# Kernel tuning notes

Measured on AMD Instinct MI355X. Metric: run time of the kernel, lower is better.

## Reference

```python
import jax, jax.numpy as jnp
import numpy as np

B, T, D, N, H = 1, 256, 512, 8, 64  # batch, seq, d_model, n_heads, d_head
INIT_STD = 0.02
IGNORE = -1000000.0
DUMMY_LOGIT = -1000.0


def setup_inputs() -> dict:
    key = jax.random.key(0)
    ks = jax.random.split(key, 9)
    std = INIT_STD
    inp = {
        'normalized_resid_pre': jax.random.normal(ks[0], (B, T, D), dtype=jnp.float32),
        'W_K1': jax.random.normal(ks[1], (N, D, H), dtype=jnp.float32) * std,
        'W_K2': jax.random.normal(ks[2], (N, D, H), dtype=jnp.float32) * std,
        'W_Q':  jax.random.normal(ks[3], (N, D, H), dtype=jnp.float32) * std,
        'W_V1': jax.random.normal(ks[4], (N, D, H), dtype=jnp.float32) * std,
        'W_V2': jax.random.normal(ks[5], (N, D, H), dtype=jnp.float32) * std,
        'W_Kq': jax.random.normal(ks[6], (N, H, H, H), dtype=jnp.float32) * std,
        'W_Vq': jax.random.normal(ks[7], (N, H, H, H), dtype=jnp.float32) * std,
        'W_O':  jax.random.normal(ks[8], (N, H, D), dtype=jnp.float32) * std,
        'b_K1': jnp.zeros((N, H), dtype=jnp.float32),
        'b_K2': jnp.zeros((N, H), dtype=jnp.float32),
        'b_Q':  jnp.zeros((N, H), dtype=jnp.float32),
        'b_V1': jnp.zeros((N, H), dtype=jnp.float32),
        'b_V2': jnp.zeros((N, H), dtype=jnp.float32),
        'b_O':  jnp.zeros((D,), dtype=jnp.float32),
    }
    return inp


def _trittention(x, W_K1, W_K2, W_Q, W_V1, W_V2, W_Kq, W_Vq, W_O,
                 b_K1, b_K2, b_Q, b_V1, b_V2, b_O):
    b, t, d = x.shape
    n, _, h = W_Q.shape
    proj = lambda W, bias: jnp.einsum('ndh,bpd->bpnh', W, x) + bias
    k1 = proj(W_K1, b_K1)  # (b, t, n, h)
    k2 = proj(W_K2, b_K2)
    q  = proj(W_Q,  b_Q)
    v1 = proj(W_V1, b_V1)
    v2 = proj(W_V2, b_V2)

    # bilinear value over pairs of positions: (b, n, h, s, t) -> flatten (s t)
    v = jnp.einsum('bsni,btnj,nijh->bnhst', v1, v2, W_Vq)
    v = v.reshape(b, n, h, t * t)

    # cubic scores: (b, n, s, t, r) with s=k1 pos, t=k2 pos, r=query pos
    step1 = jnp.einsum('brnk,nijk->bnrij', q, W_Kq)
    step2 = jnp.einsum('bnrij,btnj->bnrit', step1, k2)
    attn = jnp.einsum('bnrit,bsni->bnstr', step2, k1)

    # causal + ordering mask (order_attn=True, attn_eq=False):
    # masked if s>=r or t>=r or s>=t
    s_idx = jnp.arange(t)[:, None, None]
    t_idx = jnp.arange(t)[None, :, None]
    r_idx = jnp.arange(t)[None, None, :]
    mask = (s_idx >= r_idx) | (t_idx >= r_idx) | (s_idx >= t_idx)
    attn = jnp.where(mask, IGNORE, attn)

    # rearrange 'b n s t r -> b n r (s t)' and scale by d_head
    attn = jnp.transpose(attn, (0, 1, 4, 2, 3)).reshape(b, n, t, t * t) / h

    # causal_attn=True: append dummy logit / zero value slot
    dummy_logit = jnp.full((b, n, t, 1), DUMMY_LOGIT, dtype=attn.dtype)
    attn = jnp.concatenate([attn, dummy_logit], axis=-1)
    dummy_value = jnp.zeros((b, n, h, 1), dtype=v.dtype)
    v = jnp.concatenate([v, dummy_value], axis=-1)

    attn = jax.nn.softmax(attn, axis=-1)
    z = jnp.einsum('bnql,bnhl->bqnh', attn, v)
    out = jnp.einsum('bpnh,nhd->bpd', z, W_O) + b_O  # sum over heads folded in
    return out


def reference(normalized_resid_pre, W_K1, W_K2, W_Q, W_V1, W_V2, W_Kq, W_Vq, W_O,
              b_K1, b_K2, b_Q, b_V1, b_V2, b_O):
    return _trittention(normalized_resid_pre, W_K1, W_K2, W_Q, W_V1, W_V2,
                        W_Kq, W_Vq, W_O, b_K1, b_K2, b_Q, b_V1, b_V2, b_O)
```

## Files before the change

kernel.cpp:

```cpp
#include <hip/hip_runtime.h>
#include <hip/hip_bf16.h>
#include <math.h>

#define TT 256
#define DD 512
#define NN 8
#define HH 64
#define PROJ 131072

typedef __attribute__((ext_vector_type(8))) short short8v;
typedef __attribute__((ext_vector_type(4))) short short4v;
typedef __attribute__((ext_vector_type(4))) float f32x4;

__device__ __forceinline__ short f2bf(float x) {
    union { float f; unsigned u; } v; v.f = x;
    unsigned r = (v.u + 0x7FFFu + ((v.u >> 16) & 1u)) >> 16;
    return (short)r;
}

#define LGKM0 asm volatile("s_waitcnt lgkmcnt(0)" ::: "memory")

#define F_NUM  0
#define F_DEN  131072
#define F_END  133120
#define S_PB   0
#define S_XB   655360
#define S_WB   786432
#define S_KQB  2097152
#define S_VQB  4194304
#define S_WOB  6291456
#define S_S1B  6553600
#define S_AB   14942208
#define S_GB   23330816

__global__ __launch_bounds__(256) void prep_kernel(
    const float* __restrict__ x, const float* __restrict__ W_Kq,
    const float* __restrict__ W0, const float* __restrict__ W1,
    const float* __restrict__ W2, const float* __restrict__ W3,
    const float* __restrict__ W4, const float* __restrict__ Vq,
    const float* __restrict__ WO, short* __restrict__ sb, float* __restrict__ fz)
{
    __shared__ float plds[64 * 129];
    int b = blockIdx.x;
    int tid = threadIdx.x;
    if (b < 1024) {
        int i = b * 256 + tid;
        const float4 f0 = *(const float4*)(W_Kq + (size_t)i * 8);
        const float4 f1 = *(const float4*)(W_Kq + (size_t)i * 8 + 4);
        short8v o;
        o[0]=f2bf(f0.x); o[1]=f2bf(f0.y); o[2]=f2bf(f0.z); o[3]=f2bf(f0.w);
        o[4]=f2bf(f1.x); o[5]=f2bf(f1.y); o[6]=f2bf(f1.z); o[7]=f2bf(f1.w);
        *(short8v*)(sb + S_KQB + (size_t)i * 8) = o;
    } else if (b < 1088) {
        int i = (b - 1024) * 256 + tid;
        const float4 f0 = *(const float4*)(x + (size_t)i * 8);
        const float4 f1 = *(const float4*)(x + (size_t)i * 8 + 4);
        short8v o;
        o[0]=f2bf(f0.x); o[1]=f2bf(f0.y); o[2]=f2bf(f0.z); o[3]=f2bf(f0.w);
        o[4]=f2bf(f1.x); o[5]=f2bf(f1.y); o[6]=f2bf(f1.z); o[7]=f2bf(f1.w);
        *(short8v*)(sb + S_XB + (size_t)i * 8) = o;
    } else if (b < 1128) {
        int pn = b - 1088; int p = pn >> 3, n = pn & 7;
        const float* Wp = (p==0)?W0:(p==1)?W1:(p==2)?W2:(p==3)?W3:W4;
        const float* src = Wp + (size_t)n * DD * HH;
        short* dst = sb + S_WB + (size_t)pn * HH * DD;
        for (int d0 = 0; d0 < DD; d0 += 64) {
            __syncthreads();
            for (int it = 0; it < 16; ++it) {
                int m = it * 256 + tid;
                int dl = m >> 6, h = m & 63;
                plds[h * 65 + dl] = src[(size_t)(d0 + dl) * 64 + h];
            }
            __syncthreads();
            int h = tid >> 2, seg = tid & 3;
            short8v o0, o1;
            #pragma unroll
            for (int e = 0; e < 8; ++e) o0[e] = f2bf(plds[h * 65 + seg * 16 + e]);
            #pragma unroll
            for (int e = 0; e < 8; ++e) o1[e] = f2bf(plds[h * 65 + seg * 16 + 8 + e]);
            *(short8v*)(dst + (size_t)h * DD + d0 + seg * 16) = o0;
            *(short8v*)(dst + (size_t)h * DD + d0 + seg * 16 + 8) = o1;
        }
    } else if (b < 1640) {
        int bb = b - 1128; int n = bb >> 6, i = bb & 63;
        const float* src = Vq + (size_t)(n * 64 + i) * 4096;
        for (int it = 0; it < 16; ++it) {
            int m = it * 256 + tid;
            int j = m >> 6, h = m & 63;
            plds[h * 65 + j] = src[(size_t)j * 64 + h];
        }
        __syncthreads();
        int h = tid >> 2, seg = tid & 3;
        short8v o0, o1;
        #pragma unroll
        for (int e = 0; e < 8; ++e) o0[e] = f2bf(plds[h * 65 + seg * 16 + e]);
        #pragma unroll
        for (int e = 0; e < 8; ++e) o1[e] = f2bf(plds[h * 65 + seg * 16 + 8 + e]);
        short* dst = sb + S_VQB + (size_t)n * 262144 + (size_t)h * 4096 + i * 64 + seg * 16;
        *(short8v*)dst = o0;
        *(short8v*)(dst + 8) = o1;
    } else if (b < 1672) {
        int bb = b - 1640; int dc = bb & 7, nhc = bb >> 3;
        for (int it = 0; it < 32; ++it) {
            int m = it * 256 + tid;
            int nhl = m >> 6, dl = m & 63;
            plds[dl * 129 + nhl] = WO[(size_t)(nhc * 128 + nhl) * 512 + dc * 64 + dl];
        }
        __syncthreads();
        for (int it = 0; it < 4; ++it) {
            int m = it * 256 + tid;
            int dl = m >> 4, seg = m & 15;
            short8v o;
            #pragma unroll
            for (int e = 0; e < 8; ++e) o[e] = f2bf(plds[dl * 129 + seg * 8 + e]);
            *(short8v*)(sb + S_WOB + (size_t)(dc * 64 + dl) * 512 + nhc * 128 + seg * 8) = o;
        }
    } else {
        int i = (b - 1672) * 1024 + tid * 4;
        *(float4*)(fz + i) = make_float4(0.f, 0.f, 0.f, 0.f);
    }
}

__global__ __launch_bounds__(512) void proj_kernel(
    const short* __restrict__ xb, const short* __restrict__ Wb,
    const float* __restrict__ bK1, const float* __restrict__ bK2,
    const float* __restrict__ bQ,  const float* __restrict__ bV1,
    const float* __restrict__ bV2, short* __restrict__ Pb) {
    int p = blockIdx.x, n = blockIdx.y, mhalf = blockIdx.z;
    int wv = threadIdx.x >> 6, lane = threadIdx.x & 63, g = lane >> 4, c = lane & 15;
    __shared__ short wlds[64 * 520];
    __shared__ short sbuf[8][16 * 72];
    const short* wsrc = Wb + (size_t)(p * 8 + n) * HH * DD;
    for (int it = 0; it < 8; ++it) {
        int idx = it * 512 + threadIdx.x;
        int h = idx >> 6, seg = idx & 63;
        *(short8v*)(&wlds[h * 520 + seg * 8]) = *(const short8v*)(wsrc + (size_t)h * DD + seg * 8);
    }
    __syncthreads();
    int mt = mhalf * 8 + wv;
    f32x4 acc[4];
    #pragma unroll
    for (int ct = 0; ct < 4; ++ct) acc[ct] = (f32x4){0.f, 0.f, 0.f, 0.f};
    for (int ks = 0; ks < 16; ++ks) {
        short8v a = *(const short8v*)(xb + (size_t)(mt * 16 + c) * DD + ks * 32 + g * 8);
        #pragma unroll
        for (int ct = 0; ct < 4; ++ct) {
            short8v b = *(const short8v*)(&wlds[(ct * 16 + c) * 520 + ks * 32 + g * 8]);
            acc[ct] = __builtin_amdgcn_mfma_f32_16x16x32_bf16(a, b, acc[ct], 0, 0, 0);
        }
    }
    const float* bp = (p == 0) ? bK1 : (p == 1) ? bK2 : (p == 2) ? bQ : (p == 3) ? bV1 : bV2;
    short* sbw = &sbuf[wv][0];
    #pragma unroll
    for (int ct = 0; ct < 4; ++ct) {
        float bias = bp[n * 64 + ct * 16 + c];
        #pragma unroll
        for (int m = 0; m < 4; ++m)
            sbw[(g * 4 + m) * 72 + ct * 16 + c] = f2bf(acc[ct][m] + bias);
    }
    LGKM0;
    int rl = lane & 15, sg = lane >> 4;
    short8v o0 = *(const short8v*)(&sbw[rl * 72 + sg * 16]);
    short8v o1 = *(const short8v*)(&sbw[rl * 72 + sg * 16 + 8]);
    short* dst = Pb + (size_t)p * PROJ + (size_t)(n * 256 + mt * 16 + rl) * 64 + sg * 16;
    *(short8v*)dst = o0;
    *(short8v*)(dst + 8) = o1;
}

__global__ __launch_bounds__(256) void bgemm_kernel(
    const short* __restrict__ A0, const short* __restrict__ B0, short* __restrict__ O0,
    const short* __restrict__ A1, const short* __restrict__ B1, short* __restrict__ O1) {
    int mt = blockIdx.x, n = blockIdx.y, z = blockIdx.z;
    const short* A = (z < 4) ? A0 : A1;
    const short* B = (z < 4) ? B0 : B1;
    short* out = (z < 4) ? O0 : O1;
    int cgq = z & 3;
    int wv = threadIdx.x >> 6, lane = threadIdx.x & 63, g = lane >> 4, c = lane & 15;
    __shared__ short sbuf[4][16 * 72];
    short* sbw = &sbuf[wv][0];
    const short* abase = A + ((size_t)n * 256 + mt * 16 + c) * 64 + g * 8;
    short8v a0 = *(const short8v*)abase;
    short8v a1 = *(const short8v*)(abase + 32);
    for (int cg = cgq * 16 + wv; cg < cgq * 16 + 16; cg += 4) {
        f32x4 acc[4];
        #pragma unroll
        for (int jt = 0; jt < 4; ++jt) acc[jt] = (f32x4){0.f, 0.f, 0.f, 0.f};
        const short* bb = B + ((size_t)n * 4096 + cg * 64) * 64;
        #pragma unroll
        for (int jt = 0; jt < 4; ++jt) {
            short8v b0 = *(const short8v*)(bb + (size_t)(jt * 16 + c) * 64 + g * 8);
            short8v b1 = *(const short8v*)(bb + (size_t)(jt * 16 + c) * 64 + g * 8 + 32);
            acc[jt] = __builtin_amdgcn_mfma_f32_16x16x32_bf16(a0, b0, acc[jt], 0, 0, 0);
            acc[jt] = __builtin_amdgcn_mfma_f32_16x16x32_bf16(a1, b1, acc[jt], 0, 0, 0);
        }
        LGKM0;
        #pragma unroll
        for (int jt = 0; jt < 4; ++jt)
            #pragma unroll
            for (int m = 0; m < 4; ++m)
                sbw[(g * 4 + m) * 72 + jt * 16 + c] = f2bf(acc[jt][m]);
        LGKM0;
        int rl = lane & 15, sg = lane >> 4;
        short8v o0 = *(const short8v*)(&sbw[rl * 72 + sg * 16]);
        short8v o1 = *(const short8v*)(&sbw[rl * 72 + sg * 16 + 8]);
        short* dst = out + ((size_t)n * 256 + mt * 16 + rl) * 4096 + cg * 64 + sg * 16;
        *(short8v*)dst = o0;
        *(short8v*)(dst + 8) = o1;
    }
}

__global__ __launch_bounds__(256) void gmat_kernel(const short* __restrict__ S1b,
                                                   const short* __restrict__ K2b,
                                                   short* __restrict__ G) {
    int bid = blockIdx.x;
    int n = bid & 7;
    int tt = (bid >> 3) & 15;
    int rq = bid >> 7;
    int wv = threadIdx.x >> 6, lane = threadIdx.x & 63, g = lane >> 4, c = lane & 15;
    int t0 = tt * 16;
    __shared__ short sbuf[4][16 * 68];
    short* sbw = &sbuf[wv][0];
    const short* abase = K2b + ((size_t)n * TT + t0 + c) * 64 + g * 8;
    short8v a0 = *(const short8v*)abase;
    short8v a1 = *(const short8v*)(abase + 32);
    for (int r = t0 + rq * 4 + wv; r < 256; r += 16) {
        const short* bb = S1b + ((size_t)(n * 256 + r) * 64) * 64;
        f32x4 acc[4];
        #pragma unroll
        for (int it = 0; it < 4; ++it) {
            short8v b0 = *(const short8v*)(bb + (size_t)(it * 16 + c) * 64 + g * 8);
            short8v b1 = *(const short8v*)(bb + (size_t)(it * 16 + c) * 64 + g * 8 + 32);
            acc[it] = (f32x4){0.f, 0.f, 0.f, 0.f};
            acc[it] = __builtin_amdgcn_mfma_f32_16x16x32_bf16(a0, b0, acc[it], 0, 0, 0);
            acc[it] = __builtin_amdgcn_mfma_f32_16x16x32_bf16(a1, b1, acc[it], 0, 0, 0);
        }
        LGKM0;
        #pragma unroll
        for (int it = 0; it < 4; ++it)
            #pragma unroll
            for (int m = 0; m < 4; ++m)
                sbw[(g * 4 + m) * 68 + it * 16 + c] = f2bf(acc[it][m]);
        LGKM0;
        int trow = lane >> 2, seg = (lane & 3) * 16;
        short8v o0 = *(const short8v*)(&sbw[trow * 68 + seg]);
        short8v o1 = *(const short8v*)(&sbw[trow * 68 + seg + 8]);
        short* dst = G + (((size_t)(n * TT + t0 + trow)) * TT + r) * 64 + seg;
        *(short8v*)dst = o0;
        *(short8v*)(dst + 8) = o1;
    }
}

__global__ __launch_bounds__(1024) void attn_kernel(
    const short* __restrict__ K1b, const short* __restrict__ V1b,
    const short* __restrict__ Gm, const short* __restrict__ Ab,
    float* __restrict__ num, float* __restrict__ den)
{
    int bid = blockIdx.x;
    int n = bid & 7;
    int rest = bid >> 3;
    int pair = rest >> 2;
    int sig = rest & 3;
    int tid = threadIdx.x;
    int wv = tid >> 6, lane = tid & 63, g = lane >> 4, c = lane & 15;

    __shared__ short k1lds[64 * 72];
    __shared__ short v1lds[64 * 72];
    __shared__ short u_lds[2][64 * 68];

    int t0H = (31 - pair) * 8;
    int stmaxK = (t0H + 6) >> 4;
    int cntK = (stmaxK >= sig) ? ((stmaxK - sig) >> 2) + 1 : 0;
    for (int idx = tid; idx < cntK * 128; idx += 1024) {
        int row = idx >> 3, seg = idx & 7;
        int s = (sig + (row >> 4) * 4) * 16 + (row & 15);
        *(short8v*)(&k1lds[row * 72 + seg * 8]) =
            *(const short8v*)(K1b + ((size_t)n * TT + s) * 64 + seg * 8);
        *(short8v*)(&v1lds[row * 72 + seg * 8]) =
            *(const short8v*)(V1b + ((size_t)n * TT + s) * 64 + seg * 8);
    }
    __syncthreads();

    f32x4 numacc[4];
    #pragma unroll
    for (int b = 0; b < 4; ++b) numacc[b] = (f32x4){0.f, 0.f, 0.f, 0.f};
    float denacc = 0.f;
    int rt = wv;
    int ubuf = 0;

    for (int part = 0; part < 2; ++part) {
        int t0 = part ? t0H : pair * 8;
        for (int th = 0; th < 8; ++th) {
            int t = t0 + th;
            if (t < 1 || t > 254) continue;
            int rt_start = (t + 1) >> 4;
            int stmaxU = (t - 1) >> 4;
            int cntU = (stmaxU >= sig) ? ((stmaxU - sig) >> 2) + 1 : 0;
            if (cntU == 0) continue;

            bool valid = (rt >= rt_start);
            short8v gf0, gf1;
            if (valid) {
                const short* gb = Gm + (((size_t)(n * TT + t) * TT) + rt * 16 + c) * 64 + g * 8;
                gf0 = *(const short8v*)gb;
                gf1 = *(const short8v*)(gb + 32);
            }

            short* uw = &u_lds[ubuf][0];
            if (wv < cntU * 4) {
                int loc = wv >> 2, hs = wv & 3;
                const short* vr = &v1lds[(loc * 16 + c) * 72 + g * 8];
                short8v vf0 = *(const short8v*)vr;
                short8v vf1 = *(const short8v*)(vr + 32);
                const short* ar = Ab + (size_t)(n * TT + t) * 4096 + (hs * 16 + c) * 64 + g * 8;
                short8v ab0 = *(const short8v*)ar;
                short8v ab1 = *(const short8v*)(ar + 32);
                f32x4 ucc = (f32x4){0.f, 0.f, 0.f, 0.f};
                ucc = __builtin_amdgcn_mfma_f32_16x16x32_bf16(vf0, ab0, ucc, 0, 0, 0);
                ucc = __builtin_amdgcn_mfma_f32_16x16x32_bf16(vf1, ab1, ucc, 0, 0, 0);
                short4v uo;
                #pragma unroll
                for (int m = 0; m < 4; ++m) uo[m] = f2bf(ucc[m]);
                *(short4v*)(&uw[(hs * 16 + c) * 68 + loc * 16 + g * 4]) = uo;
            }
            __syncthreads();
            ubuf ^= 1;

            if (valid) {
                int r = rt * 16 + c;
                for (int loc = 0; loc < cntU; ++loc) {
                    int s_base = (sig + loc * 4) * 16;
                    const short* kr = &k1lds[(loc * 16 + c) * 72 + g * 8];
                    short8v af0 = *(const short8v*)kr;
                    short8v af1 = *(const short8v*)(kr + 32);
                    f32x4 lg = (f32x4){0.f, 0.f, 0.f, 0.f};
                    lg = __builtin_amdgcn_mfma_f32_16x16x32_bf16(af0, gf0, lg, 0, 0, 0);
                    lg = __builtin_amdgcn_mfma_f32_16x16x32_bf16(af1, gf1, lg, 0, 0, 0);
                    short4v eb;
                    float dsum = 0.f;
                    #pragma unroll
                    for (int m = 0; m < 4; ++m) {
                        int s = s_base + g * 4 + m;
                        float e = (s < t && r > t) ? __expf(lg[m] * 0.015625f) : 0.f;
                        dsum += e;
                        eb[m] = f2bf(e);
                    }
                    denacc += dsum;
                    #pragma unroll
                    for (int hs = 0; hs < 4; ++hs) {
                        short4v ub = *(const short4v*)(&uw[(hs * 16 + c) * 68 + loc * 16 + g * 4]);
                        numacc[hs] = __builtin_amdgcn_mfma_f32_16x16x16bf16_1k(eb, ub, numacc[hs], 0, 0, 0);
                    }
                }
            }
        }
    }

    if (__any(denacc != 0.f)) {
        float v = denacc;
        v += __shfl_xor(v, 16);
        v += __shfl_xor(v, 32);
        if (lane < 16) atomicAdd(&den[n * TT + rt * 16 + lane], v);
        #pragma unroll
        for (int hs = 0; hs < 4; ++hs)
            #pragma unroll
            for (int m = 0; m < 4; ++m)
                atomicAdd(&num[((size_t)(n * TT + rt * 16 + g * 4 + m)) * 64 + hs * 16 + c],
                          numacc[hs][m]);
    }
}

__global__ __launch_bounds__(512) void out_kernel(const float* __restrict__ num,
                                                  const float* __restrict__ den,
                                                  const short* __restrict__ WOb,
                                                  const float* __restrict__ bO,
                                                  float* __restrict__ out) {
    int mt = blockIdx.x & 15, dq = blockIdx.x >> 4;
    int wv = threadIdx.x >> 6, lane = threadIdx.x & 63, g = lane >> 4, c = lane & 15;
    int dt0 = dq * 16 + wv * 2;
    int t = mt * 16 + c;
    f32x4 acc[2];
    acc[0] = (f32x4){0.f, 0.f, 0.f, 0.f};
    acc[1] = (f32x4){0.f, 0.f, 0.f, 0.f};
    for (int ks = 0; ks < 16; ++ks) {
        int nh = ks * 32 + g * 8;
        int nn = nh >> 6, h = nh & 63;
        float dv = den[nn * 256 + t];
        float rcp = (dv > 0.f) ? 1.f / dv : 0.f;
        const float* np = num + ((size_t)(nn * 256 + t) * 64 + h);
        float4 f0 = *(const float4*)np;
        float4 f1 = *(const float4*)(np + 4);
        short8v a;
        a[0]=f2bf(f0.x*rcp); a[1]=f2bf(f0.y*rcp); a[2]=f2bf(f0.z*rcp); a[3]=f2bf(f0.w*rcp);
        a[4]=f2bf(f1.x*rcp); a[5]=f2bf(f1.y*rcp); a[6]=f2bf(f1.z*rcp); a[7]=f2bf(f1.w*rcp);
        #pragma unroll
        for (int u = 0; u < 2; ++u) {
            short8v b = *(const short8v*)(WOb + (size_t)((dt0 + u) * 16 + c) * 512 + ks * 32 + g * 8);
            acc[u] = __builtin_amdgcn_mfma_f32_16x16x32_bf16(a, b, acc[u], 0, 0, 0);
        }
    }
    #pragma unroll
    for (int u = 0; u < 2; ++u) {
        int d = (dt0 + u) * 16 + c;
        float bias = bO[d];
        #pragma unroll
        for (int m = 0; m < 4; ++m)
            out[(size_t)(mt * 16 + g * 4 + m) * 512 + d] = acc[u][m] + bias;
    }
}

extern "C" void kernel_launch(void* const* d_in, const int* in_sizes, int n_in,
                              void* d_out, int out_size, void* d_ws, size_t ws_size,
                              hipStream_t stream) {
    const float* x    = (const float*)d_in[0];
    const float* W_K1 = (const float*)d_in[1];
    const float* W_K2 = (const float*)d_in[2];
    const float* W_Q  = (const float*)d_in[3];
    const float* W_V1 = (const float*)d_in[4];
    const float* W_V2 = (const float*)d_in[5];
    const float* W_Kq = (const float*)d_in[6];
    const float* W_Vq = (const float*)d_in[7];
    const float* W_O  = (const float*)d_in[8];
    const float* b_K1 = (const float*)d_in[9];
    const float* b_K2 = (const float*)d_in[10];
    const float* b_Q  = (const float*)d_in[11];
    const float* b_V1 = (const float*)d_in[12];
    const float* b_V2 = (const float*)d_in[13];
    const float* b_O  = (const float*)d_in[14];
    float* ws = (float*)d_ws;
    short* sb = (short*)(ws + F_END);
    float* out = (float*)d_out;

    prep_kernel<<<1802, 256, 0, stream>>>(x, W_Kq, W_K1, W_K2, W_Q, W_V1, W_V2,
                                          W_Vq, W_O, sb, ws + F_NUM);

    proj_kernel<<<dim3(5, 8, 2), 512, 0, stream>>>(sb + S_XB, sb + S_WB,
                                                   b_K1, b_K2, b_Q, b_V1, b_V2, sb + S_PB);

    bgemm_kernel<<<dim3(16, 8, 8), 256, 0, stream>>>(
        sb + S_PB + 2 * PROJ, sb + S_KQB, sb + S_S1B,
        sb + S_PB + 4 * PROJ, sb + S_VQB, sb + S_AB);

    gmat_kernel<<<512, 256, 0, stream>>>(sb + S_S1B, sb + S_PB + 1 * PROJ, sb + S_GB);

    attn_kernel<<<512, 1024, 0, stream>>>(sb + S_PB, sb + S_PB + 3 * PROJ,
                                          sb + S_GB, sb + S_AB,
                                          ws + F_NUM, ws + F_DEN);

    out_kernel<<<32, 512, 0, stream>>>(ws + F_NUM, ws + F_DEN, sb + S_WOB, b_O, out);
}
```

Baseline: 146.5 us.

## Batch U-tile computation for eight t values per part to cut barriers

Instead of computing one U tile per t and syncing the block every iteration, each part now computes U tiles for all eight t values into an enlarged shared buffer, with two barriers per part. The V1 fragment is hoisted out of the loop since each wave's loc index is fixed. This removes per-t __syncthreads stalls and lets the score/accumulate loop run without barriers. In exchange shared memory for U grows about fourfold, which may reduce occupancy, and it adds a hard sync between the U phase and the attention phase.

```diff
diff --git a/kernel.cpp b/kernel.cpp
--- a/kernel.cpp
+++ b/kernel.cpp
@@ -265,7 +265,7 @@
 
     __shared__ short k1lds[64 * 72];
     __shared__ short v1lds[64 * 72];
-    __shared__ short u_lds[2][64 * 68];
+    __shared__ short u_lds[8][64][68];
 
     int t0H = (31 - pair) * 8;
     int stmaxK = (t0H + 6) >> 4;
@@ -285,71 +285,69 @@
     for (int b = 0; b < 4; ++b) numacc[b] = (f32x4){0.f, 0.f, 0.f, 0.f};
     float denacc = 0.f;
     int rt = wv;
-    int ubuf = 0;
+    int lU = wv >> 2, hU = wv & 3;
+
+    const short* vr = &v1lds[(lU * 16 + c) * 72 + g * 8];
+    short8v vf0 = *(const short8v*)vr;
+    short8v vf1 = *(const short8v*)(vr + 32);
 
     for (int part = 0; part < 2; ++part) {
         int t0 = part ? t0H : pair * 8;
-        for (int th = 0; th < 8; ++th) {
-            int t = t0 + th;
+
+        __syncthreads();
+        for (int tl = 0; tl < 8; ++tl) {
+            int t = t0 + tl;
+            int stm = (t - 1) >> 4;
+            int cntU = (t >= 1 && stm >= sig) ? ((stm - sig) >> 2) + 1 : 0;
+            if (lU >= cntU) continue;
+            const short* ar = Ab + (size_t)(n * TT + t) * 4096 + (hU * 16 + c) * 64 + g * 8;
+            short8v ab0 = *(const short8v*)ar;
+            short8v ab1 = *(const short8v*)(ar + 32);
+            f32x4 ucc = (f32x4){0.f, 0.f, 0.f, 0.f};
+            ucc = __builtin_amdgcn_mfma_f32_16x16x32_bf16(vf0, ab0, ucc, 0, 0, 0);
+            ucc = __builtin_amdgcn_mfma_f32_16x16x32_bf16(vf1, ab1, ucc, 0, 0, 0);
+            short4v uo;
+            #pragma unroll
+            for (int m = 0; m < 4; ++m) uo[m] = f2bf(ucc[m]);
+            *(short4v*)(&u_lds[tl][hU * 16 + c][lU * 16 + g * 4]) = uo;
+        }
+        __syncthreads();
+
+        for (int tl = 0; tl < 8; ++tl) {
+            int t = t0 + tl;
             if (t < 1 || t > 254) continue;
             int rt_start = (t + 1) >> 4;
             int stmaxU = (t - 1) >> 4;
             int cntU = (stmaxU >= sig) ? ((stmaxU - sig) >> 2) + 1 : 0;
-            if (cntU == 0) continue;
-
-            bool valid = (rt >= rt_start);
-            short8v gf0, gf1;
-            if (valid) {
-                const short* gb = Gm + (((size_t)(n * TT + t) * TT) + rt * 16 + c) * 64 + g * 8;
-                gf0 = *(const short8v*)gb;
-                gf1 = *(const short8v*)(gb + 32);
-            }
-
-            short* uw = &u_lds[ubuf][0];
-            if (wv < cntU * 4) {
-                int loc = wv >> 2, hs = wv & 3;
-                const short* vr = &v1lds[(loc * 16 + c) * 72 + g * 8];
-                short8v vf0 = *(const short8v*)vr;
-                short8v vf1 = *(const short8v*)(vr + 32);
-                const short* ar = Ab + (size_t)(n * TT + t) * 4096 + (hs * 16 + c) * 64 + g * 8;
-                short8v ab0 = *(const short8v*)ar;
-                short8v ab1 = *(const short8v*)(ar + 32);
-                f32x4 ucc = (f32x4){0.f, 0.f, 0.f, 0.f};
-                ucc = __builtin_amdgcn_mfma_f32_16x16x32_bf16(vf0, ab0, ucc, 0, 0, 0);
-                ucc = __builtin_amdgcn_mfma_f32_16x16x32_bf16(vf1, ab1, ucc, 0, 0, 0);
-                short4v uo;
+            if (cntU == 0 || rt < rt_start) continue;
+
+            const short* gb = Gm + (((size_t)(n * TT + t) * TT) + rt * 16 + c) * 64 + g * 8;
+            short8v gf0 = *(const short8v*)gb;
+            short8v gf1 = *(const short8v*)(gb + 32);
+            int r = rt * 16 + c;
+
+            for (int loc = 0; loc < cntU; ++loc) {
+                int s_base = (sig + loc * 4) * 16;
+                const short* kr = &k1lds[(loc * 16 + c) * 72 + g * 8];
+                short8v af0 = *(const short8v*)kr;
+                short8v af1 = *(const short8v*)(kr + 32);
+                f32x4 lg = (f32x4){0.f, 0.f, 0.f, 0.f};
+                lg = __builtin_amdgcn_mfma_f32_16x16x32_bf16(af0, gf0, lg, 0, 0, 0);
+                lg = __builtin_amdgcn_mfma_f32_16x16x32_bf16(af1, gf1, lg, 0, 0, 0);
+                short4v eb;
+                float dsum = 0.f;
                 #pragma unroll
-                for (int m = 0; m < 4; ++m) uo[m] = f2bf(ucc[m]);
-                *(short4v*)(&uw[(hs * 16 + c) * 68 + loc * 16 + g * 4]) = uo;
-            }
-            __syncthreads();
-            ubuf ^= 1;
-
-            if (valid) {
-                int r = rt * 16 + c;
-                for (int loc = 0; loc < cntU; ++loc) {
-                    int s_base = (sig + loc * 4) * 16;
-                    const short* kr = &k1lds[(loc * 16 + c) * 72 + g * 8];
-                    short8v af0 = *(const short8v*)kr;
-                    short8v af1 = *(const short8v*)(kr + 32);
-                    f32x4 lg = (f32x4){0.f, 0.f, 0.f, 0.f};
-                    lg = __builtin_amdgcn_mfma_f32_16x16x32_bf16(af0, gf0, lg, 0, 0, 0);
-                    lg = __builtin_amdgcn_mfma_f32_16x16x32_bf16(af1, gf1, lg, 0, 0, 0);
-                    short4v eb;
-                    float dsum = 0.f;
-                    #pragma unroll
-                    for (int m = 0; m < 4; ++m) {
-                        int s = s_base + g * 4 + m;
-                        float e = (s < t && r > t) ? __expf(lg[m] * 0.015625f) : 0.f;
-                        dsum += e;
-                        eb[m] = f2bf(e);
-                    }
-                    denacc += dsum;
-                    #pragma unroll
-                    for (int hs = 0; hs < 4; ++hs) {
-                        short4v ub = *(const short4v*)(&uw[(hs * 16 + c) * 68 + loc * 16 + g * 4]);
-                        numacc[hs] = __builtin_amdgcn_mfma_f32_16x16x16bf16_1k(eb, ub, numacc[hs], 0, 0, 0);
-                    }
+                for (int m = 0; m < 4; ++m) {
+                    int s = s_base + g * 4 + m;
+                    float e = (s < t && r > t) ? __expf(lg[m] * 0.015625f) : 0.f;
+                    dsum += e;
+                    eb[m] = f2bf(e);
+                }
+                denacc += dsum;
+                #pragma unroll
+                for (int hs = 0; hs < 4; ++hs) {
+                    short4v ub = *(const short4v*)(&u_lds[tl][hs * 16 + c][loc * 16 + g * 4]);
+                    numacc[hs] = __builtin_amdgcn_mfma_f32_16x16x16bf16_1k(eb, ub, numacc[hs], 0, 0, 0);
                 }
             }
         }
```

After: 152.3 us. 4.0% more time.
